# Optimization experiments

Hardware: AMD Instinct MI355X
Metric: run time of the kernel (lower is better)

## Reference

```python
import jax, jax.numpy as jnp
import numpy as np
import math

SCALE = math.sqrt(256.0)

def setup_inputs() -> dict:
    key = jax.random.key(0)
    k1, k2, k3, k4, k5 = jax.random.split(key, 5)
    B, C, T, D = 8, 80, 2048, 256
    bound = 1.0 / math.sqrt(C)
    x = jax.random.normal(k1, (B, C, T), dtype=jnp.float32)
    Wk = jax.random.uniform(k2, (D, C), minval=-bound, maxval=bound, dtype=jnp.float32)
    bk = jax.random.uniform(k3, (D,), minval=-bound, maxval=bound, dtype=jnp.float32)
    Wq = jax.random.uniform(k4, (D, C), minval=-bound, maxval=bound, dtype=jnp.float32)
    bq = jax.random.uniform(k5, (D,), minval=-bound, maxval=bound, dtype=jnp.float32)
    return {"x": x, "Wk": Wk, "bk": bk, "Wq": Wq, "bq": bq}

def reference(x, Wk, bk, Wq, bq):
    # x: [B, C=80, T]; work in time-major layout [B, T, C]
    xt = jnp.swapaxes(x, 1, 2)                      # [B, T, C]
    K = xt @ Wk.T + bk                              # [B, T, 256]
    Q = xt @ Wq.T + bq                              # [B, T, 256]
    # softmax over last dim (dim=2 in torch) of K Q^T / sqrt(256)
    att = jax.nn.softmax(jnp.einsum('bid,bjd->bij', K, Q) / SCALE, axis=2)
    # original per-timestep loop is exactly att @ xt (values = raw input, no V proj)
    out = jnp.einsum('bij,bjc->bic', att, xt)       # [B, T, C]
    return jnp.swapaxes(out, 1, 2)                  # [B, C, T]
```

## Files before the change

kernel.cpp:

```cpp
#include <hip/hip_runtime.h>
#include <hip/hip_bf16.h>
#include <math.h>

typedef __bf16 bf16;
typedef __bf16 bf16x8 __attribute__((ext_vector_type(8)));
typedef float  f32x4  __attribute__((ext_vector_type(4)));
typedef float  f32x16 __attribute__((ext_vector_type(16)));
typedef uint32_t u32x2 __attribute__((ext_vector_type(2)));
typedef uint32_t u32x4 __attribute__((ext_vector_type(4)));

#define MFMA16(a, b, c) __builtin_amdgcn_mfma_f32_16x16x32_bf16((a), (b), (c), 0, 0, 0)
#define MFMA32(a, b, c) __builtin_amdgcn_mfma_f32_32x32x16_bf16((a), (b), (c), 0, 0, 0)

typedef const uint32_t __attribute__((address_space(1)))* gq_t;
typedef uint32_t __attribute__((address_space(3)))* lq_t;

constexpr int B_ = 8, C_ = 80, T_ = 2048, D_ = 256;
constexpr int NS = 4;
constexpr float LOG2E_16 = 0.090169989f;

static __device__ inline uint32_t pkbf(float lo, float hi) {
  bf16 l = (bf16)lo, h = (bf16)hi;
  uint16_t lb = __builtin_bit_cast(uint16_t, l), hb = __builtin_bit_cast(uint16_t, h);
  return (uint32_t)lb | ((uint32_t)hb << 16);
}

constexpr int VF_TILE = 3 * 2 * 2 * 32 * 8;

__global__ __launch_bounds__(256) void wconv_kernel(
    const float* __restrict__ Wk, const float* __restrict__ bk,
    const float* __restrict__ Wq, const float* __restrict__ bq,
    bf16* __restrict__ Wbf)
{
  const int mat = blockIdx.x, d = threadIdx.x;
  const float* W    = mat ? Wq : Wk;
  const float* bias = mat ? bq : bk;
  bf16* row = Wbf + (size_t)(mat * 256 + d) * 96;
  const float bv = bias[d];
  #pragma unroll
  for (int c8 = 0; c8 < 12; ++c8) {
    bf16x8 o;
    #pragma unroll
    for (int e = 0; e < 8; ++e) {
      int c = c8 * 8 + e;
      float v = (c < 80) ? W[d * C_ + c] : (c == 80 ? bv : 0.f);
      o[e] = (bf16)v;
    }
    *reinterpret_cast<bf16x8*>(row + c8 * 8) = o;
  }
}

__global__ __launch_bounds__(256) void proj_kernel(
    const float* __restrict__ x,
    const bf16* __restrict__ Wbf,
    bf16* __restrict__ Kb,
    bf16* __restrict__ Qb,
    bf16* __restrict__ Vf)
{
  const int t0   = blockIdx.x * 32;
  const int b    = blockIdx.y;
  const int tid  = threadIdx.x;
  const int w    = tid >> 6;
  const int lane = tid & 63;
  const int h    = lane >> 4;
  const int lr   = lane & 15;

  const float* xb = x + (size_t)b * C_ * T_;

  {
    bf16* vout = Vf + (size_t)(b * 64 + blockIdx.x) * VF_TILE;
    #pragma unroll
    for (int g = 0; g < 2; ++g) {
      int f = tid + g * 256;
      if (f < 384) {
        int il2 = f & 31, hi2 = (f >> 5) & 1, kj2 = (f >> 6) & 1, cb2 = f >> 7;
        int c = cb2 * 32 + il2;
        bf16x8 o;
        if (c < 80) {
          const float* sp = xb + (size_t)c * T_ + t0 + kj2 * 16 + hi2 * 8;
          f32x4 v0 = *reinterpret_cast<const f32x4*>(sp);
          f32x4 v1 = *reinterpret_cast<const f32x4*>(sp + 4);
          #pragma unroll
          for (int e = 0; e < 4; ++e) { o[e] = (bf16)v0[e]; o[e + 4] = (bf16)v1[e]; }
        } else {
          #pragma unroll
          for (int e = 0; e < 8; ++e) o[e] = (bf16)0.f;
        }
        *reinterpret_cast<bf16x8*>(vout + f * 8) = o;
      }
    }
  }

  bf16x8 afrag[2][3];
  #pragma unroll
  for (int ib = 0; ib < 2; ++ib) {
    int t = t0 + ib * 16 + lr;
    #pragma unroll
    for (int ks = 0; ks < 3; ++ks) {
      bf16x8 v;
      #pragma unroll
      for (int e = 0; e < 8; ++e) {
        int c = ks * 32 + h * 8 + e;
        float val;
        if (c < 80)       val = xb[c * T_ + t];
        else if (c == 80) val = 1.0f;
        else              val = 0.0f;
        v[e] = (bf16)val;
      }
      afrag[ib][ks] = v;
    }
  }

  const int nb0 = w * 4;
  #pragma unroll
  for (int mat = 0; mat < 2; ++mat) {
    bf16* outp = mat ? Qb : Kb;

    f32x4 acc[2][4];
    #pragma unroll
    for (int ib = 0; ib < 2; ++ib)
      #pragma unroll
      for (int nb = 0; nb < 4; ++nb)
        acc[ib][nb] = f32x4{0.f, 0.f, 0.f, 0.f};

    #pragma unroll
    for (int nb = 0; nb < 4; ++nb) {
      int d = (nb0 + nb) * 16 + lr;
      const bf16* wrow = Wbf + (size_t)(mat * 256 + d) * 96;
      #pragma unroll
      for (int ks = 0; ks < 3; ++ks) {
        bf16x8 bv = *reinterpret_cast<const bf16x8*>(wrow + ks * 32 + h * 8);
        #pragma unroll
        for (int ib = 0; ib < 2; ++ib)
          acc[ib][nb] = MFMA16(afrag[ib][ks], bv, acc[ib][nb]);
      }
    }

    #pragma unroll
    for (int ib = 0; ib < 2; ++ib)
      #pragma unroll
      for (int nb = 0; nb < 4; ++nb) {
        int d = (nb0 + nb) * 16 + lr;
        #pragma unroll
        for (int r = 0; r < 4; ++r) {
          int t = t0 + ib * 16 + h * 4 + r;
          outp[(size_t)(b * T_ + t) * D_ + d] = (bf16)acc[ib][nb][r];
        }
      }
  }
}

__global__ __launch_bounds__(256, 2) void attn_kernel(
    const bf16* __restrict__ Kb,
    const bf16* __restrict__ Qb,
    const bf16* __restrict__ Vf,
    float* __restrict__ Opart,
    float* __restrict__ mpart,
    float* __restrict__ lpart)
{
  constexpr int BN = 64, NSTG = T_ / BN;
  constexpr int STG_PER = NSTG / NS;
  __shared__ bf16 qlds[2][BN * D_];

  const int flat = blockIdx.x;
  const int b    = flat & 7;
  const int rem  = flat >> 3;
  const int it   = rem & 15;
  const int s    = rem >> 4;
  const int i0   = it * 128;

  const int tid  = threadIdx.x;
  const int w    = tid >> 6;
  const int lane = tid & 63;
  const int il   = lane & 31;
  const int hi   = lane >> 5;
  const int iw   = i0 + w * 32;

  const bf16* Kbase = Kb + (size_t)b * T_ * D_;
  const bf16* Qbase = Qb + (size_t)b * T_ * D_;
  const bf16* Vbase = Vf + (size_t)b * 64 * VF_TILE;

  bf16x8 kf[16];
  {
    const bf16* kp = Kbase + (size_t)(iw + il) * D_ + hi * 8;
    #pragma unroll
    for (int ks = 0; ks < 16; ++ks)
      kf[ks] = *reinterpret_cast<const bf16x8*>(kp + ks * 16);
  }

  f32x16 oacc[3];
  #pragma unroll
  for (int cb = 0; cb < 3; ++cb)
    #pragma unroll
    for (int r = 0; r < 16; ++r) oacc[cb][r] = 0.f;
  float m_run = -INFINITY, l_run = 0.f;

  const int st0 = s * STG_PER;
  const int off = (it & 3) * 2;
  auto smap = [&](int t) { return st0 + ((t - st0 + off) & (STG_PER - 1)); };

  auto stage = [&](int st, int buf) {
    #pragma unroll
    for (int q = 0; q < 8; ++q) {
      int f = tid + 256 * q;
      int j = f >> 5, c = f & 31;
      const bf16* src = Qbase + (size_t)(st * BN + j) * D_ + ((c ^ (j & 31)) << 3);
      __builtin_amdgcn_global_load_lds((gq_t)src,
          (lq_t)&qlds[buf][(q * 256 + w * 64) * 8], 16, 0, 0);
    }
  };

  stage(smap(st0), 0);
  asm volatile("s_waitcnt vmcnt(0)" ::: "memory");
  __syncthreads();

  int cur = 0;
  for (int t = st0; t < st0 + STG_PER; ++t, cur ^= 1) {
    const int st = smap(t);
    if (t + 1 < st0 + STG_PER) stage(smap(t + 1), cur ^ 1);

    #pragma unroll
    for (int hf = 0; hf < 2; ++hf) {
      const int j32 = st * 2 + hf;

      const bf16* vt = Vbase + (size_t)j32 * VF_TILE + lane * 8;
      bf16x8 vf[3][2];
      #pragma unroll
      for (int cb = 0; cb < 3; ++cb)
        #pragma unroll
        for (int kj = 0; kj < 2; ++kj)
          vf[cb][kj] = *reinterpret_cast<const bf16x8*>(vt + (cb * 2 + kj) * 512);

      f32x16 sacc;
      #pragma unroll
      for (int r = 0; r < 16; ++r) sacc[r] = 0.f;
      __builtin_amdgcn_s_setprio(1);
      #pragma unroll
      for (int ks = 0; ks < 16; ++ks) {
        bf16x8 qa = *reinterpret_cast<const bf16x8*>(
            &qlds[cur][(hf * 32 + il) * 256 + (((hi + 2 * ks) ^ il) << 3)]);
        sacc = MFMA32(qa, kf[ks], sacc);
      }
      __builtin_amdgcn_s_setprio(0);

      float p16[16];
      #pragma unroll
      for (int r = 0; r < 16; ++r) p16[r] = sacc[r];
      float t0 = fmaxf(fmaxf(p16[0],  p16[1]),  p16[2]);
      float t1 = fmaxf(fmaxf(p16[3],  p16[4]),  p16[5]);
      float t2 = fmaxf(fmaxf(p16[6],  p16[7]),  p16[8]);
      float t3 = fmaxf(fmaxf(p16[9],  p16[10]), p16[11]);
      float t4 = fmaxf(fmaxf(p16[12], p16[13]), p16[14]);
      float mx = fmaxf(fmaxf(fmaxf(t0, t1), t2),
                       fmaxf(fmaxf(t3, t4), p16[15]));
      mx = fmaxf(mx, __shfl_xor(mx, 32));

      if (!__all(mx <= m_run + 48.f)) {
        float mnew  = fmaxf(m_run, mx);
        float alpha = exp2f((m_run - mnew) * LOG2E_16);
        m_run = mnew;
        l_run *= alpha;
        #pragma unroll
        for (int cb = 0; cb < 3; ++cb)
          #pragma unroll
          for (int r = 0; r < 16; ++r) oacc[cb][r] *= alpha;
      }
      #pragma unroll
      for (int r = 0; r < 16; ++r)
        p16[r] = exp2f((p16[r] - m_run) * LOG2E_16);
      {
        float s0 = (p16[0] + p16[1]) + (p16[2] + p16[3]);
        float s1 = (p16[4] + p16[5]) + (p16[6] + p16[7]);
        float s2 = (p16[8] + p16[9]) + (p16[10] + p16[11]);
        float s3 = (p16[12] + p16[13]) + (p16[14] + p16[15]);
        l_run += (s0 + s1) + (s2 + s3);
      }

      uint32_t a0 = pkbf(p16[0],  p16[1]),  a1 = pkbf(p16[2],  p16[3]);
      uint32_t c0 = pkbf(p16[4],  p16[5]),  c1 = pkbf(p16[6],  p16[7]);
      uint32_t a2 = pkbf(p16[8],  p16[9]),  a3 = pkbf(p16[10], p16[11]);
      uint32_t c2 = pkbf(p16[12], p16[13]), c3 = pkbf(p16[14], p16[15]);
      u32x2 w0 = __builtin_amdgcn_permlane32_swap(a0, c0, false, false);
      u32x2 w1 = __builtin_amdgcn_permlane32_swap(a1, c1, false, false);
      u32x2 w2 = __builtin_amdgcn_permlane32_swap(a2, c2, false, false);
      u32x2 w3 = __builtin_amdgcn_permlane32_swap(a3, c3, false, false);
      u32x4 pb0 = { w0[0], w1[0], w0[1], w1[1] };
      u32x4 pb1 = { w2[0], w3[0], w2[1], w3[1] };
      bf16x8 pbf0 = __builtin_bit_cast(bf16x8, pb0);
      bf16x8 pbf1 = __builtin_bit_cast(bf16x8, pb1);

      __builtin_amdgcn_s_setprio(1);
      #pragma unroll
      for (int cb = 0; cb < 3; ++cb) {
        oacc[cb] = MFMA32(vf[cb][0], pbf0, oacc[cb]);
        oacc[cb] = MFMA32(vf[cb][1], pbf1, oacc[cb]);
      }
      __builtin_amdgcn_s_setprio(0);
    }

    asm volatile("s_waitcnt vmcnt(0)" ::: "memory");
    __syncthreads();
  }

  l_run += __shfl_xor(l_run, 32);

  float* ob = Opart + (size_t)(s * B_ + b) * C_ * T_;
  #pragma unroll
  for (int cb = 0; cb < 3; ++cb)
    #pragma unroll
    for (int r = 0; r < 16; ++r) {
      if (cb < 2 || r < 8) {
        int c = cb * 32 + (r & 3) + 8 * (r >> 2) + 4 * hi;
        ob[(size_t)c * T_ + iw + il] = oacc[cb][r];
      }
    }
  if (lane < 32) {
    mpart[(size_t)(s * B_ + b) * T_ + iw + il] = m_run;
    lpart[(size_t)(s * B_ + b) * T_ + iw + il] = l_run;
  }
}

__global__ __launch_bounds__(256) void merge_kernel(
    const float* __restrict__ Opart,
    const float* __restrict__ mpart,
    const float* __restrict__ lpart,
    float* __restrict__ out)
{
  const int b      = blockIdx.y;
  const int tid    = threadIdx.x;
  const int slot   = tid & 15;
  const int cstrip = tid >> 4;
  const int t4     = blockIdx.x * 64 + slot * 4;

  f32x4 m[NS], e[NS];
  f32x4 mmax;
  #pragma unroll
  for (int s2 = 0; s2 < NS; ++s2)
    m[s2] = *reinterpret_cast<const f32x4*>(&mpart[(size_t)(s2 * B_ + b) * T_ + t4]);
  #pragma unroll
  for (int r = 0; r < 4; ++r) {
    mmax[r] = m[0][r];
    #pragma unroll
    for (int s2 = 1; s2 < NS; ++s2) mmax[r] = fmaxf(mmax[r], m[s2][r]);
  }
  f32x4 lsum = f32x4{0.f, 0.f, 0.f, 0.f};
  #pragma unroll
  for (int s2 = 0; s2 < NS; ++s2) {
    f32x4 lv = *reinterpret_cast<const f32x4*>(&lpart[(size_t)(s2 * B_ + b) * T_ + t4]);
    #pragma unroll
    for (int r = 0; r < 4; ++r) e[s2][r] = exp2f((m[s2][r] - mmax[r]) * LOG2E_16);
    lsum += e[s2] * lv;
  }
  f32x4 inv;
  #pragma unroll
  for (int r = 0; r < 4; ++r) inv[r] = 1.0f / lsum[r];

  #pragma unroll
  for (int cc = 0; cc < 5; ++cc) {
    const int c = cstrip * 5 + cc;
    f32x4 acc = f32x4{0.f, 0.f, 0.f, 0.f};
    #pragma unroll
    for (int s2 = 0; s2 < NS; ++s2)
      acc += *reinterpret_cast<const f32x4*>(
                 &Opart[((size_t)(s2 * B_ + b) * C_ + c) * T_ + t4]) * e[s2];
    *reinterpret_cast<f32x4*>(&out[((size_t)b * C_ + c) * T_ + t4]) = acc * inv;
  }
}

extern "C" void kernel_launch(void* const* d_in, const int* in_sizes, int n_in,
                              void* d_out, int out_size, void* d_ws, size_t ws_size,
                              hipStream_t stream) {
  (void)in_sizes; (void)n_in; (void)out_size; (void)ws_size;
  const float* x  = (const float*)d_in[0];
  const float* Wk = (const float*)d_in[1];
  const float* bk = (const float*)d_in[2];
  const float* Wq = (const float*)d_in[3];
  const float* bq = (const float*)d_in[4];
  float* out = (float*)d_out;

  char* ws = (char*)d_ws;
  const size_t MB = 1024 * 1024;
  bf16*  Kb    = (bf16*)(ws);
  bf16*  Qb    = (bf16*)(ws + 8 * MB);
  bf16*  Vf    = (bf16*)(ws + 16 * MB);
  bf16*  Wbf   = (bf16*)(ws + 19 * MB);
  float* Opart = (float*)(ws + 20 * MB);
  float* mpart = (float*)(ws + 42 * MB);
  float* lpart = (float*)(ws + 43 * MB);

  dim3 blk(256);
  wconv_kernel<<<dim3(2), blk, 0, stream>>>(Wk, bk, Wq, bq, Wbf);
  dim3 g1(T_ / 32, B_);
  proj_kernel<<<g1, blk, 0, stream>>>(x, Wbf, Kb, Qb, Vf);
  attn_kernel<<<dim3(16 * NS * B_), blk, 0, stream>>>(Kb, Qb, Vf, Opart, mpart, lpart);
  dim3 g3(T_ / 64, B_);
  merge_kernel<<<g3, blk, 0, stream>>>(Opart, mpart, lpart, out);
}
```

Before: 64.59 us.

## Issue both QK^T halves before softmax and widen merge kernel grid

The attention inner loop now computes both 32-row QK^T score blocks back to back before doing softmax and PV for each. The second V fragment load is deferred until after the first softmax. This lets MFMA work overlap with softmax VALU work and delays V register pressure, at the cost of holding two score accumulators live. Separately, the merge kernel now gives each block 16 timesteps instead of 64, with each thread covering one or two channels. That raises the number of blocks, and the m/l reduction is recomputed per thread with less reuse.

```diff
diff --git a/kernel.cpp b/kernel.cpp
--- a/kernel.cpp
+++ b/kernel.cpp
@@ -210,6 +210,84 @@
     }
   };
 
+  auto qkt = [&](int buf, int hf, f32x16& sc) {
+    #pragma unroll
+    for (int r = 0; r < 16; ++r) sc[r] = 0.f;
+    __builtin_amdgcn_s_setprio(1);
+    #pragma unroll
+    for (int ks = 0; ks < 16; ++ks) {
+      bf16x8 qa = *reinterpret_cast<const bf16x8*>(
+          &qlds[buf][(hf * 32 + il) * 256 + (((hi + 2 * ks) ^ il) << 3)]);
+      sc = MFMA32(qa, kf[ks], sc);
+    }
+    __builtin_amdgcn_s_setprio(0);
+  };
+
+  auto smax_pv = [&](f32x16& sacc, bf16x8 (&vf)[3][2]) {
+    float p16[16];
+    #pragma unroll
+    for (int r = 0; r < 16; ++r) p16[r] = sacc[r];
+    float q0 = fmaxf(fmaxf(p16[0],  p16[1]),  p16[2]);
+    float q1 = fmaxf(fmaxf(p16[3],  p16[4]),  p16[5]);
+    float q2 = fmaxf(fmaxf(p16[6],  p16[7]),  p16[8]);
+    float q3 = fmaxf(fmaxf(p16[9],  p16[10]), p16[11]);
+    float q4 = fmaxf(fmaxf(p16[12], p16[13]), p16[14]);
+    float mx = fmaxf(fmaxf(fmaxf(q0, q1), q2),
+                     fmaxf(fmaxf(q3, q4), p16[15]));
+    mx = fmaxf(mx, __shfl_xor(mx, 32));
+
+    if (!__all(mx <= m_run + 48.f)) {
+      float mnew  = fmaxf(m_run, mx);
+      float alpha = exp2f((m_run - mnew) * LOG2E_16);
+      m_run = mnew;
+      l_run *= alpha;
+      #pragma unroll
+      for (int cb = 0; cb < 3; ++cb)
+        #pragma unroll
+        for (int r = 0; r < 16; ++r) oacc[cb][r] *= alpha;
+    }
+    #pragma unroll
+    for (int r = 0; r < 16; ++r)
+      p16[r] = exp2f((p16[r] - m_run) * LOG2E_16);
+    {
+      float s0 = (p16[0] + p16[1]) + (p16[2] + p16[3]);
+      float s1 = (p16[4] + p16[5]) + (p16[6] + p16[7]);
+      float s2 = (p16[8] + p16[9]) + (p16[10] + p16[11]);
+      float s3 = (p16[12] + p16[13]) + (p16[14] + p16[15]);
+      l_run += (s0 + s1) + (s2 + s3);
+    }
+
+    uint32_t a0 = pkbf(p16[0],  p16[1]),  a1 = pkbf(p16[2],  p16[3]);
+    uint32_t c0 = pkbf(p16[4],  p16[5]),  c1 = pkbf(p16[6],  p16[7]);
+    uint32_t a2 = pkbf(p16[8],  p16[9]),  a3 = pkbf(p16[10], p16[11]);
+    uint32_t c2 = pkbf(p16[12], p16[13]), c3 = pkbf(p16[14], p16[15]);
+    u32x2 w0 = __builtin_amdgcn_permlane32_swap(a0, c0, false, false);
+    u32x2 w1 = __builtin_amdgcn_permlane32_swap(a1, c1, false, false);
+    u32x2 w2 = __builtin_amdgcn_permlane32_swap(a2, c2, false, false);
+    u32x2 w3 = __builtin_amdgcn_permlane32_swap(a3, c3, false, false);
+    u32x4 pb0 = { w0[0], w1[0], w0[1], w1[1] };
+    u32x4 pb1 = { w2[0], w3[0], w2[1], w3[1] };
+    bf16x8 pbf0 = __builtin_bit_cast(bf16x8, pb0);
+    bf16x8 pbf1 = __builtin_bit_cast(bf16x8, pb1);
+
+    __builtin_amdgcn_s_setprio(1);
+    #pragma unroll
+    for (int cb = 0; cb < 3; ++cb) {
+      oacc[cb] = MFMA32(vf[cb][0], pbf0, oacc[cb]);
+      oacc[cb] = MFMA32(vf[cb][1], pbf1, oacc[cb]);
+    }
+    __builtin_amdgcn_s_setprio(0);
+  };
+
+  auto vload = [&](int j32, bf16x8 (&vf)[3][2]) {
+    const bf16* vt = Vbase + (size_t)j32 * VF_TILE + lane * 8;
+    #pragma unroll
+    for (int cb = 0; cb < 3; ++cb)
+      #pragma unroll
+      for (int kj = 0; kj < 2; ++kj)
+        vf[cb][kj] = *reinterpret_cast<const bf16x8*>(vt + (cb * 2 + kj) * 512);
+  };
+
   stage(smap(st0), 0);
   asm volatile("s_waitcnt vmcnt(0)" ::: "memory");
   __syncthreads();
@@ -219,84 +297,16 @@
     const int st = smap(t);
     if (t + 1 < st0 + STG_PER) stage(smap(t + 1), cur ^ 1);
 
-    #pragma unroll
-    for (int hf = 0; hf < 2; ++hf) {
-      const int j32 = st * 2 + hf;
-
-      const bf16* vt = Vbase + (size_t)j32 * VF_TILE + lane * 8;
-      bf16x8 vf[3][2];
-      #pragma unroll
-      for (int cb = 0; cb < 3; ++cb)
-        #pragma unroll
-        for (int kj = 0; kj < 2; ++kj)
-          vf[cb][kj] = *reinterpret_cast<const bf16x8*>(vt + (cb * 2 + kj) * 512);
-
-      f32x16 sacc;
-      #pragma unroll
-      for (int r = 0; r < 16; ++r) sacc[r] = 0.f;
-      __builtin_amdgcn_s_setprio(1);
-      #pragma unroll
-      for (int ks = 0; ks < 16; ++ks) {
-        bf16x8 qa = *reinterpret_cast<const bf16x8*>(
-            &qlds[cur][(hf * 32 + il) * 256 + (((hi + 2 * ks) ^ il) << 3)]);
-        sacc = MFMA32(qa, kf[ks], sacc);
-      }
-      __builtin_amdgcn_s_setprio(0);
-
-      float p16[16];
-      #pragma unroll
-      for (int r = 0; r < 16; ++r) p16[r] = sacc[r];
-      float t0 = fmaxf(fmaxf(p16[0],  p16[1]),  p16[2]);
-      float t1 = fmaxf(fmaxf(p16[3],  p16[4]),  p16[5]);
-      float t2 = fmaxf(fmaxf(p16[6],  p16[7]),  p16[8]);
-      float t3 = fmaxf(fmaxf(p16[9],  p16[10]), p16[11]);
-      float t4 = fmaxf(fmaxf(p16[12], p16[13]), p16[14]);
-      float mx = fmaxf(fmaxf(fmaxf(t0, t1), t2),
-                       fmaxf(fmaxf(t3, t4), p16[15]));
-      mx = fmaxf(mx, __shfl_xor(mx, 32));
-
-      if (!__all(mx <= m_run + 48.f)) {
-        float mnew  = fmaxf(m_run, mx);
-        float alpha = exp2f((m_run - mnew) * LOG2E_16);
-        m_run = mnew;
-        l_run *= alpha;
-        #pragma unroll
-        for (int cb = 0; cb < 3; ++cb)
-          #pragma unroll
-          for (int r = 0; r < 16; ++r) oacc[cb][r] *= alpha;
-      }
-      #pragma unroll
-      for (int r = 0; r < 16; ++r)
-        p16[r] = exp2f((p16[r] - m_run) * LOG2E_16);
-      {
-        float s0 = (p16[0] + p16[1]) + (p16[2] + p16[3]);
-        float s1 = (p16[4] + p16[5]) + (p16[6] + p16[7]);
-        float s2 = (p16[8] + p16[9]) + (p16[10] + p16[11]);
-        float s3 = (p16[12] + p16[13]) + (p16[14] + p16[15]);
-        l_run += (s0 + s1) + (s2 + s3);
-      }
-
-      uint32_t a0 = pkbf(p16[0],  p16[1]),  a1 = pkbf(p16[2],  p16[3]);
-      uint32_t c0 = pkbf(p16[4],  p16[5]),  c1 = pkbf(p16[6],  p16[7]);
-      uint32_t a2 = pkbf(p16[8],  p16[9]),  a3 = pkbf(p16[10], p16[11]);
-      uint32_t c2 = pkbf(p16[12], p16[13]), c3 = pkbf(p16[14], p16[15]);
-      u32x2 w0 = __builtin_amdgcn_permlane32_swap(a0, c0, false, false);
-      u32x2 w1 = __builtin_amdgcn_permlane32_swap(a1, c1, false, false);
-      u32x2 w2 = __builtin_amdgcn_permlane32_swap(a2, c2, false, false);
-      u32x2 w3 = __builtin_amdgcn_permlane32_swap(a3, c3, false, false);
-      u32x4 pb0 = { w0[0], w1[0], w0[1], w1[1] };
-      u32x4 pb1 = { w2[0], w3[0], w2[1], w3[1] };
-      bf16x8 pbf0 = __builtin_bit_cast(bf16x8, pb0);
-      bf16x8 pbf1 = __builtin_bit_cast(bf16x8, pb1);
-
-      __builtin_amdgcn_s_setprio(1);
-      #pragma unroll
-      for (int cb = 0; cb < 3; ++cb) {
-        oacc[cb] = MFMA32(vf[cb][0], pbf0, oacc[cb]);
-        oacc[cb] = MFMA32(vf[cb][1], pbf1, oacc[cb]);
-      }
-      __builtin_amdgcn_s_setprio(0);
-    }
+    bf16x8 vf0[3][2], vf1[3][2];
+    vload(st * 2, vf0);
+
+    f32x16 sacc0, sacc1;
+    qkt(cur, 0, sacc0);
+    qkt(cur, 1, sacc1);
+
+    smax_pv(sacc0, vf0);
+    vload(st * 2 + 1, vf1);
+    smax_pv(sacc1, vf1);
 
     asm volatile("s_waitcnt vmcnt(0)" ::: "memory");
     __syncthreads();
@@ -326,11 +336,11 @@
     const float* __restrict__ lpart,
     float* __restrict__ out)
 {
-  const int b      = blockIdx.y;
-  const int tid    = threadIdx.x;
-  const int slot   = tid & 15;
-  const int cstrip = tid >> 4;
-  const int t4     = blockIdx.x * 64 + slot * 4;
+  const int b    = blockIdx.y;
+  const int tid  = threadIdx.x;
+  const int slot = tid & 3;
+  const int c1   = tid >> 2;
+  const int t4   = blockIdx.x * 16 + slot * 4;
 
   f32x4 m[NS], e[NS];
   f32x4 mmax;
@@ -356,14 +366,16 @@
   for (int r = 0; r < 4; ++r) inv[r] = 1.0f / lsum[r];
 
   #pragma unroll
-  for (int cc = 0; cc < 5; ++cc) {
-    const int c = cstrip * 5 + cc;
-    f32x4 acc = f32x4{0.f, 0.f, 0.f, 0.f};
-    #pragma unroll
-    for (int s2 = 0; s2 < NS; ++s2)
-      acc += *reinterpret_cast<const f32x4*>(
-                 &Opart[((size_t)(s2 * B_ + b) * C_ + c) * T_ + t4]) * e[s2];
-    *reinterpret_cast<f32x4*>(&out[((size_t)b * C_ + c) * T_ + t4]) = acc * inv;
+  for (int pass = 0; pass < 2; ++pass) {
+    const int c = c1 + pass * 64;
+    if (pass == 0 || c1 < 16) {
+      f32x4 acc = f32x4{0.f, 0.f, 0.f, 0.f};
+      #pragma unroll
+      for (int s2 = 0; s2 < NS; ++s2)
+        acc += *reinterpret_cast<const f32x4*>(
+                   &Opart[((size_t)(s2 * B_ + b) * C_ + c) * T_ + t4]) * e[s2];
+      *reinterpret_cast<f32x4*>(&out[((size_t)b * C_ + c) * T_ + t4]) = acc * inv;
+    }
   }
 }
 
@@ -393,6 +405,6 @@
   dim3 g1(T_ / 32, B_);
   proj_kernel<<<g1, blk, 0, stream>>>(x, Wbf, Kb, Qb, Vf);
   attn_kernel<<<dim3(16 * NS * B_), blk, 0, stream>>>(Kb, Qb, Vf, Opart, mpart, lpart);
-  dim3 g3(T_ / 64, B_);
+  dim3 g3(T_ / 16, B_);
   merge_kernel<<<g3, blk, 0, stream>>>(Opart, mpart, lpart, out);
 }
```

Result: slower. 68.76 us (+6.4%).
